# Optimization experiments

Measured on AMD Instinct MI355X. Metric: run time of the kernel, lower is better.

The kernel has to match this reference:

```python
import jax, jax.numpy as jnp
import numpy as np

WS = 8        # window_size
NH = 16       # num_heads

def setup_inputs() -> dict:
    key = jax.random.key(0)
    ks = jax.random.split(key, 6)
    B, H, W, C = 16, 64, 64, 512
    nW = (H // WS) * (W // WS)
    return {
        "x": jax.random.normal(ks[0], (B, H * W, C), jnp.float32),
        "qkv_w": jax.random.normal(ks[1], (3 * C, C), jnp.float32) * 0.02,
        "qkv_b": jax.random.normal(ks[2], (3 * C,), jnp.float32) * 0.02,
        "proj_w": jax.random.normal(ks[3], (C, C), jnp.float32) * 0.02,
        "proj_b": jax.random.normal(ks[4], (C,), jnp.float32) * 0.02,
        "attn_mask": jax.random.normal(ks[5], (nW, WS * WS, WS * WS), jnp.float32),
        "H": H,
        "W": W,
    }

def reference(x, qkv_w, qkv_b, proj_w, proj_b, attn_mask, H, W):
    B, N, C = x.shape
    ws = WS
    hd = C // NH
    scale = hd ** (-0.5)
    x_img = x.reshape(B, H, W, C)
    pad_h = (ws - H % ws) % ws
    pad_w = (ws - W % ws) % ws
    if pad_h > 0 or pad_w > 0:
        x_img = jnp.pad(x_img, ((0, 0), (0, pad_h), (0, pad_w), (0, 0)))
    Hp, Wp = H + pad_h, W + pad_w
    nW = (Hp // ws) * (Wp // ws)
    # window partition: [B*nW, ws*ws, C]
    x_win = x_img.reshape(B, Hp // ws, ws, Wp // ws, ws, C)
    x_win = x_win.transpose(0, 1, 3, 2, 4, 5).reshape(B * nW, ws * ws, C)
    # fused qkv projection (torch Linear: y = x @ W^T + b)
    qkv = x_win @ qkv_w.T + qkv_b
    qkv = qkv.reshape(B * nW, ws * ws, 3, NH, hd).transpose(2, 0, 3, 1, 4)
    q, k, v = qkv[0], qkv[1], qkv[2]  # each [B*nW, NH, ws*ws, hd]
    attn = jnp.einsum('bhqd,bhkd->bhqk', q, k) * scale
    if attn_mask is not None:
        attn = attn.reshape(B, nW, NH, ws * ws, ws * ws)
        attn = attn + attn_mask[None, :, None, :, :]
        attn = attn.reshape(B * nW, NH, ws * ws, ws * ws)
    attn = jax.nn.softmax(attn, axis=-1)
    out = jnp.einsum('bhqk,bhkd->bhqd', attn, v)
    out = out.transpose(0, 2, 1, 3).reshape(B * nW, ws * ws, C)
    out = out @ proj_w.T + proj_b
    # window reverse
    out = out.reshape(B, Hp // ws, Wp // ws, ws, ws, C)
    out = out.transpose(0, 1, 3, 2, 4, 5).reshape(B, Hp, Wp, C)
    out = out[:, :H, :W, :].reshape(B, H * W, C)
    return out
```

## Files before the change

kernel.cpp:

```cpp
#include <hip/hip_runtime.h>


typedef unsigned short u16;
typedef unsigned int u32;
typedef __attribute__((ext_vector_type(8))) u16 u16x8;
typedef __attribute__((ext_vector_type(8))) short short8;
typedef __attribute__((ext_vector_type(4))) float f32x4;

__device__ __forceinline__ u16 f2bf(float f) {
    u32 u = __float_as_uint(f);
    u += 0x7fffu + ((u >> 16) & 1u);
    return (u16)(u >> 16);
}

__device__ __forceinline__ f32x4 MFMA(u16x8 a, u16x8 b, f32x4 c) {
    return __builtin_amdgcn_mfma_f32_16x16x32_bf16(
        __builtin_bit_cast(short8, a), __builtin_bit_cast(short8, b), c, 0, 0, 0);
}

__device__ __forceinline__ void gload16(const void* g, void* l) {
    __builtin_amdgcn_global_load_lds(
        (const __attribute__((address_space(1))) void*)g,
        (__attribute__((address_space(3))) void*)l, 16, 0, 0);
}

__device__ __forceinline__ int win2img(int r) {
    int b = r >> 12;
    int w = (r >> 6) & 63;
    int t = r & 63;
    int img = (((w >> 3) << 3) + (t >> 3)) * 64 + ((w & 7) << 3) + (t & 7);
    return (b << 12) + img;
}

__device__ __forceinline__ u16x8 cvt8(const float* src) {
    float4 a = *(const float4*)src;
    float4 b = *(const float4*)(src + 4);
    u16x8 t;
    t[0] = f2bf(a.x); t[1] = f2bf(a.y); t[2] = f2bf(a.z); t[3] = f2bf(a.w);
    t[4] = f2bf(b.x); t[5] = f2bf(b.y); t[6] = f2bf(b.z); t[7] = f2bf(b.w);
    return t;
}

__global__ __launch_bounds__(256)
void conv_f2b(const float* __restrict__ in, u16* __restrict__ out, int n8) {
    int u = blockIdx.x * 256 + threadIdx.x;
    if (u >= n8) return;
    *(u16x8*)(out + (size_t)u * 8) = cvt8(in + (size_t)u * 8);
}

__global__ __launch_bounds__(256)
void conv_permute_x(const float* __restrict__ x, u16* __restrict__ xw) {
    int u = blockIdx.x * 256 + threadIdx.x;
    int r = u >> 6;
    int c = (u & 63) << 3;
    int g = win2img(r);
    *(u16x8*)(xw + (size_t)r * 512 + c) = cvt8(x + (size_t)g * 512 + c);
}

template<bool PERM_OUT, bool OUT_F32>
__global__ __launch_bounds__(512, 1)
void gemm8p(const u16* __restrict__ A, const u16* __restrict__ Wt,
            const float* __restrict__ bias, void* __restrict__ C,
            int NB, int Nfull)
{
    __shared__ char lds[131072];

    const int nwg = gridDim.x;
    const int q   = nwg >> 3;
    const int wg  = ((int)blockIdx.x & 7) * q + ((int)blockIdx.x >> 3);
    const int m0  = (wg / NB) * 256;
    const int n0  = (wg % NB) * 256;

    const int tid  = threadIdx.x;
    const int lane = tid & 63;
    const int wv   = tid >> 6;
    const int wm128 = (wv >> 2) << 7;
    const int wn64  = (wv & 3) << 6;
    const int lr = lane & 15;
    const int lg = lane >> 4;

    const int srow = tid >> 3;
    const int gcol = (((tid & 7) ^ (srow & 7)) << 4);
    const char* Ag = (const char*)A + (((size_t)(m0 + srow)) << 10) + gcol;
    const char* Bg = (const char*)Wt + (((size_t)(n0 + srow)) << 10) + gcol;
    const u32 stb = (u32)tid << 4;

    const int colx = (lr & 7) << 4;
    const u32 aro = (u32)(wm128 + lr) << 7;
    const u32 bro = (u32)(wn64 + lr) << 7;

    f32x4 acc[8][4] = {};
    u16x8 af[4], bf[4];

#define STG(buf, OP, h, kt) do {                                              \
    const char* g_ = (OP) ? Bg : Ag;                                          \
    char* d_ = lds + (buf) * 65536 + (OP) * 32768 + (h) * 16384 + stb;        \
    gload16(g_ + ((size_t)((h) * 128) << 10) + ((kt) << 7), d_);              \
    gload16(g_ + ((size_t)((h) * 128 + 64) << 10) + ((kt) << 7), d_ + 8192);  \
} while (0)

#define RDA(buf, h, s) do {                                                   \
    _Pragma("unroll") for (int j_ = 0; j_ < 4; ++j_)                          \
        af[j_] = *(const u16x8*)(lds + (buf) * 65536 + aro                    \
                   + (((h) * 4 + j_) << 11) + ((((s) << 6) + (lg << 4)) ^ colx)); \
} while (0)

#define RDB(buf, s) do {                                                      \
    _Pragma("unroll") for (int n_ = 0; n_ < 4; ++n_)                          \
        bf[n_] = *(const u16x8*)(lds + (buf) * 65536 + 32768 + bro            \
                   + (n_ << 11) + ((((s) << 6) + (lg << 4)) ^ colx));         \
} while (0)

#define MM16(h) do {                                                          \
    __builtin_amdgcn_s_setprio(1);                                            \
    _Pragma("unroll") for (int j_ = 0; j_ < 4; ++j_)                          \
        _Pragma("unroll") for (int n_ = 0; n_ < 4; ++n_)                      \
            acc[(h) * 4 + j_][n_] = MFMA(af[j_], bf[n_], acc[(h) * 4 + j_][n_]); \
    __builtin_amdgcn_s_setprio(0);                                            \
} while (0)

#define BAR() __builtin_amdgcn_s_barrier()
#define LGK0() do { asm volatile("s_waitcnt lgkmcnt(0)" ::: "memory");        \
                    __builtin_amdgcn_sched_barrier(0); } while (0)

    STG(0, 0, 0, 0); STG(0, 0, 1, 0); STG(0, 1, 0, 0); STG(0, 1, 1, 0);
    __syncthreads();

#pragma unroll
    for (int it = 0; it < 4; ++it) {
        const int t1 = 2 * it + 1, t2 = 2 * it + 2;
        RDA(0, 0, 0); RDB(0, 0);
        STG(1, 0, 0, t1); STG(1, 1, 0, t1);
        BAR(); LGK0(); MM16(0); BAR();
        RDA(0, 1, 0);
        STG(1, 0, 1, t1); STG(1, 1, 1, t1);
        BAR(); LGK0(); MM16(1); BAR();
        RDA(0, 0, 1); RDB(0, 1);
        BAR(); LGK0(); MM16(0); BAR();
        RDA(0, 1, 1);
        BAR(); LGK0(); MM16(1);
        __syncthreads();
        RDA(1, 0, 0); RDB(1, 0);
        if (it < 3) { STG(0, 0, 0, t2); STG(0, 1, 0, t2); }
        BAR(); LGK0(); MM16(0); BAR();
        RDA(1, 1, 0);
        if (it < 3) { STG(0, 0, 1, t2); STG(0, 1, 1, t2); }
        BAR(); LGK0(); MM16(1); BAR();
        RDA(1, 0, 1); RDB(1, 1);
        BAR(); LGK0(); MM16(0); BAR();
        RDA(1, 1, 1);
        BAR(); LGK0(); MM16(1);
        __syncthreads();
    }

#undef STG
#undef RDA
#undef RDB
#undef MM16
#undef BAR
#undef LGK0

#pragma unroll
    for (int ni = 0; ni < 4; ++ni) {
        const int col = n0 + wn64 + ni * 16 + lr;
        const float bv = bias[col];
#pragma unroll
        for (int mi = 0; mi < 8; ++mi) {
#pragma unroll
            for (int r = 0; r < 4; ++r) {
                int gr = m0 + wm128 + mi * 16 + lg * 4 + r;
                if (PERM_OUT) gr = win2img(gr);
                const float v = acc[mi][ni][r] + bv;
                if constexpr (OUT_F32)
                    ((float*)C)[(size_t)gr * Nfull + col] = v;
                else
                    ((u16*)C)[(size_t)gr * Nfull + col] = f2bf(v);
            }
        }
    }
}

__global__ __launch_bounds__(256, 2)
void attn_kernel(const u16* __restrict__ qkv, const float* __restrict__ mask,
                 u16* __restrict__ attn_out)
{
    __shared__ u16 sP[4][64][72];

    const int tid  = threadIdx.x;
    const int lane = tid & 63;
    const int wv   = tid >> 6;
    const int lr   = lane & 15;
    const int lg   = lane >> 4;
    const int win  = blockIdx.x;
    const int wib  = win & 63;
    const size_t rb = (size_t)win * 64;
    const float* maskp = mask + (size_t)wib * 64 * 64;
    const float scale = 0.17677669529663687f;

    for (int hi = 0; hi < 4; ++hi) {
        const int h = hi * 4 + wv;
        const size_t hoff = (size_t)h * 32;

        u16x8 qf[4], kf[4];
#pragma unroll
        for (int mt = 0; mt < 4; ++mt) {
            const u16* rowp = qkv + (rb + mt * 16 + lr) * 1536 + hoff + lg * 8;
            qf[mt] = *(const u16x8*)rowp;
            kf[mt] = *(const u16x8*)(rowp + 512);
        }
        f32x4 s[4][4] = {};
#pragma unroll
        for (int mi = 0; mi < 4; ++mi)
#pragma unroll
            for (int ni = 0; ni < 4; ++ni)
                s[mi][ni] = MFMA(qf[mi], kf[ni], s[mi][ni]);

        float rsum[4][4];
#pragma unroll
        for (int mi = 0; mi < 4; ++mi) {
#pragma unroll
            for (int r = 0; r < 4; ++r) {
                const int qrow = mi * 16 + lg * 4 + r;
                float vv[4];
                float mx = -1e30f;
#pragma unroll
                for (int ni = 0; ni < 4; ++ni) {
                    const int kcol = ni * 16 + lr;
                    float v = s[mi][ni][r] * scale + maskp[qrow * 64 + kcol];
                    vv[ni] = v;
                    mx = fmaxf(mx, v);
                }
#pragma unroll
                for (int mk = 1; mk <= 8; mk <<= 1)
                    mx = fmaxf(mx, __shfl_xor(mx, mk, 64));
                float sum = 0.f;
#pragma unroll
                for (int ni = 0; ni < 4; ++ni) {
                    float p = __expf(vv[ni] - mx);
                    sum += p;
                    s[mi][ni][r] = p;
                }
#pragma unroll
                for (int mk = 1; mk <= 8; mk <<= 1)
                    sum += __shfl_xor(sum, mk, 64);
                rsum[mi][r] = sum;
            }
        }

        __syncthreads();
#pragma unroll
        for (int mi = 0; mi < 4; ++mi)
#pragma unroll
            for (int ni = 0; ni < 4; ++ni)
#pragma unroll
                for (int r = 0; r < 4; ++r)
                    sP[wv][mi * 16 + lg * 4 + r][ni * 16 + lr] = f2bf(s[mi][ni][r]);
        __syncthreads();

        u16x8 pf[4][2];
#pragma unroll
        for (int mt = 0; mt < 4; ++mt)
#pragma unroll
            for (int k2 = 0; k2 < 2; ++k2)
                pf[mt][k2] = *(const u16x8*)&sP[wv][mt * 16 + lr][k2 * 32 + lg * 8];

        u16x8 vf[2][2];
#pragma unroll
        for (int k2 = 0; k2 < 2; ++k2)
#pragma unroll
            for (int nt = 0; nt < 2; ++nt) {
                const u16* vp = qkv + (rb + k2 * 32 + lg * 8) * 1536 + 1024 + hoff + nt * 16 + lr;
                u16x8 tmp;
#pragma unroll
                for (int j = 0; j < 8; ++j) tmp[j] = vp[(size_t)j * 1536];
                vf[k2][nt] = tmp;
            }

        f32x4 o[4][2] = {};
#pragma unroll
        for (int mt = 0; mt < 4; ++mt)
#pragma unroll
            for (int k2 = 0; k2 < 2; ++k2)
#pragma unroll
                for (int nt = 0; nt < 2; ++nt)
                    o[mt][nt] = MFMA(pf[mt][k2], vf[k2][nt], o[mt][nt]);

#pragma unroll
        for (int mt = 0; mt < 4; ++mt)
#pragma unroll
            for (int nt = 0; nt < 2; ++nt)
#pragma unroll
                for (int r = 0; r < 4; ++r) {
                    const int row = mt * 16 + lg * 4 + r;
                    const int d = nt * 16 + lr;
                    attn_out[(rb + row) * 512 + hoff + d] =
                        f2bf(o[mt][nt][r] / rsum[mt][r]);
                }
    }
}

extern "C" void kernel_launch(void* const* d_in, const int* in_sizes, int n_in,
                              void* d_out, int out_size, void* d_ws, size_t ws_size,
                              hipStream_t stream)
{
    const float* x      = (const float*)d_in[0];
    const float* qkv_w  = (const float*)d_in[1];
    const float* qkv_b  = (const float*)d_in[2];
    const float* proj_w = (const float*)d_in[3];
    const float* proj_b = (const float*)d_in[4];
    const float* mask   = (const float*)d_in[5];
    float* out = (float*)d_out;

    const size_t WQKV  = 1536ull * 512;
    const size_t WPROJ = 512ull * 512;

    u16* wq = (u16*)d_ws;
    u16* wp = wq + WQKV;
    u16* chunk = wp + WPROJ;

    const size_t xwPB  = 4096ull * 512;
    const size_t qkvPB = 4096ull * 1536;
    const size_t attPB = 4096ull * 512;
    const size_t perBatchBytes = (xwPB + qkvPB + attPB) * 2;

    size_t avail = ws_size - (WQKV + WPROJ) * 2;
    int Bc = (int)(avail / perBatchBytes);
    if (Bc > 16) Bc = 16;
    if (Bc < 1) Bc = 1;

    u16* xw_ws  = chunk;
    u16* qkv_ws = xw_ws + (size_t)Bc * xwPB;
    u16* att_ws = qkv_ws + (size_t)Bc * qkvPB;

    conv_f2b<<<dim3((WQKV / 8 + 255) / 256), 256, 0, stream>>>(qkv_w, wq, (int)(WQKV / 8));
    conv_f2b<<<dim3((WPROJ / 8 + 255) / 256), 256, 0, stream>>>(proj_w, wp, (int)(WPROJ / 8));

    for (int b0 = 0; b0 < 16; b0 += Bc) {
        const int bc = (16 - b0) < Bc ? (16 - b0) : Bc;
        const float* xc = x + (size_t)b0 * 4096 * 512;
        float* outc = out + (size_t)b0 * 4096 * 512;

        conv_permute_x<<<dim3(bc * 1024), 256, 0, stream>>>(xc, xw_ws);
        gemm8p<false, false><<<dim3(bc * 16 * 6), 512, 0, stream>>>(
            xw_ws, wq, qkv_b, qkv_ws, 6, 1536);
        attn_kernel<<<dim3(bc * 64), 256, 0, stream>>>(qkv_ws, mask, att_ws);
        gemm8p<true, true><<<dim3(bc * 16 * 2), 512, 0, stream>>>(
            att_ws, wp, proj_b, outc, 2, 512);
    }
}
```

Before: 347.6 us.

## Restructure GEMM mainloop to 4-slot ring of BK=32 tiles with prefetch depth two

Replaces the two-buffer BK=64 staging scheme with a four-slot LDS ring of BK=32 K-tiles, prefetching two tiles ahead and using vmcnt waits instead of full __syncthreads between stages. The LDS swizzle and load layout change to 64-byte rows with a 4-way XOR. The aim is to keep more global loads in flight and cut barrier stalls around the MFMA work. In exchange it uses more, finer-grained iterations and relies on tricky vmcnt accounting, which is a correctness risk.

Measured after the change: 357.4 us. 2.8% more time.

```diff
diff --git a/kernel.cpp b/kernel.cpp
--- a/kernel.cpp
+++ b/kernel.cpp
@@ -79,36 +79,36 @@
     const int lr = lane & 15;
     const int lg = lane >> 4;
 
-    const int srow = tid >> 3;
-    const int gcol = (((tid & 7) ^ (srow & 7)) << 4);
-    const char* Ag = (const char*)A + (((size_t)(m0 + srow)) << 10) + gcol;
-    const char* Bg = (const char*)Wt + (((size_t)(n0 + srow)) << 10) + gcol;
+    const int srow = tid >> 2;
+    const int gcolb = (((tid & 3) ^ ((tid >> 3) & 3)) << 4);
+    const char* Ag = (const char*)A + (((size_t)(m0 + srow)) << 10) + gcolb;
+    const char* Bg = (const char*)Wt + (((size_t)(n0 + srow)) << 10) + gcolb;
     const u32 stb = (u32)tid << 4;
 
-    const int colx = (lr & 7) << 4;
-    const u32 aro = (u32)(wm128 + lr) << 7;
-    const u32 bro = (u32)(wn64 + lr) << 7;
+    const u32 cbyte = (u32)((lg ^ ((lr >> 1) & 3)) << 4);
+    const u32 aoff = (u32)(wm128 + lr) * 64 + cbyte;
+    const u32 boff = (u32)(wn64 + lr) * 64 + cbyte + 16384;
 
     f32x4 acc[8][4] = {};
     u16x8 af[4], bf[4];
 
-#define STG(buf, OP, h, kt) do {                                              \
-    const char* g_ = (OP) ? Bg : Ag;                                          \
-    char* d_ = lds + (buf) * 65536 + (OP) * 32768 + (h) * 16384 + stb;        \
-    gload16(g_ + ((size_t)((h) * 128) << 10) + ((kt) << 7), d_);              \
-    gload16(g_ + ((size_t)((h) * 128 + 64) << 10) + ((kt) << 7), d_ + 8192);  \
-} while (0)
-
-#define RDA(buf, h, s) do {                                                   \
+#define STG(slot, kt) do {                                                    \
+    char* d_ = lds + (slot) * 32768 + stb;                                    \
+    const size_t ko_ = (size_t)(kt) << 6;                                     \
+    gload16(Ag + ko_,                d_);                                     \
+    gload16(Ag + (128 << 10) + ko_,  d_ + 8192);                              \
+    gload16(Bg + ko_,                d_ + 16384);                             \
+    gload16(Bg + (128 << 10) + ko_,  d_ + 24576);                             \
+} while (0)
+
+#define RDA(sb, h) do {                                                       \
     _Pragma("unroll") for (int j_ = 0; j_ < 4; ++j_)                          \
-        af[j_] = *(const u16x8*)(lds + (buf) * 65536 + aro                    \
-                   + (((h) * 4 + j_) << 11) + ((((s) << 6) + (lg << 4)) ^ colx)); \
-} while (0)
-
-#define RDB(buf, s) do {                                                      \
+        af[j_] = *(const u16x8*)(lds + (sb) + aoff + (((h) * 4 + j_) << 10)); \
+} while (0)
+
+#define RDB(sb) do {                                                          \
     _Pragma("unroll") for (int n_ = 0; n_ < 4; ++n_)                          \
-        bf[n_] = *(const u16x8*)(lds + (buf) * 65536 + 32768 + bro            \
-                   + (n_ << 11) + ((((s) << 6) + (lg << 4)) ^ colx));         \
+        bf[n_] = *(const u16x8*)(lds + (sb) + boff + (n_ << 10));             \
 } while (0)
 
 #define MM16(h) do {                                                          \
@@ -120,45 +120,43 @@
 } while (0)
 
 #define BAR() __builtin_amdgcn_s_barrier()
-#define LGK0() do { asm volatile("s_waitcnt lgkmcnt(0)" ::: "memory");        \
-                    __builtin_amdgcn_sched_barrier(0); } while (0)
-
-    STG(0, 0, 0, 0); STG(0, 0, 1, 0); STG(0, 1, 0, 0); STG(0, 1, 1, 0);
-    __syncthreads();
-
-#pragma unroll
-    for (int it = 0; it < 4; ++it) {
-        const int t1 = 2 * it + 1, t2 = 2 * it + 2;
-        RDA(0, 0, 0); RDB(0, 0);
-        STG(1, 0, 0, t1); STG(1, 1, 0, t1);
-        BAR(); LGK0(); MM16(0); BAR();
-        RDA(0, 1, 0);
-        STG(1, 0, 1, t1); STG(1, 1, 1, t1);
-        BAR(); LGK0(); MM16(1); BAR();
-        RDA(0, 0, 1); RDB(0, 1);
-        BAR(); LGK0(); MM16(0); BAR();
-        RDA(0, 1, 1);
-        BAR(); LGK0(); MM16(1);
-        __syncthreads();
-        RDA(1, 0, 0); RDB(1, 0);
-        if (it < 3) { STG(0, 0, 0, t2); STG(0, 1, 0, t2); }
-        BAR(); LGK0(); MM16(0); BAR();
-        RDA(1, 1, 0);
-        if (it < 3) { STG(0, 0, 1, t2); STG(0, 1, 1, t2); }
-        BAR(); LGK0(); MM16(1); BAR();
-        RDA(1, 0, 1); RDB(1, 1);
-        BAR(); LGK0(); MM16(0); BAR();
-        RDA(1, 1, 1);
-        BAR(); LGK0(); MM16(1);
-        __syncthreads();
+#define SB0() __builtin_amdgcn_sched_barrier(0)
+#define LGK0() do { asm volatile("s_waitcnt lgkmcnt(0)" ::: "memory"); SB0(); } while (0)
+#define VMC(n) do { asm volatile("s_waitcnt vmcnt(" #n ")" ::: "memory"); } while (0)
+
+    STG(0, 0);
+    STG(1, 1);
+
+#define TILE_BODY(t_, do_stg_)  do {                                          \
+    const int slot_ = (t_) & 3;                                               \
+    const int sb_ = slot_ * 32768;                                            \
+    BAR(); SB0();                                                             \
+    RDA(sb_, 0); RDB(sb_);                                                    \
+    if (do_stg_) STG(((t_) + 2) & 3, (t_) + 2);                               \
+    LGK0(); MM16(0); BAR();                                                   \
+    RDA(sb_, 1);                                                              \
+    LGK0(); MM16(1);                                                          \
+} while (0)
+
+#pragma unroll 2
+    for (int t = 0; t < 14; ++t) {
+        VMC(4);
+        TILE_BODY(t, 1);
     }
+    VMC(4); TILE_BODY(14, 0);
+    VMC(0); TILE_BODY(15, 0);
 
 #undef STG
 #undef RDA
 #undef RDB
 #undef MM16
 #undef BAR
+#undef SB0
 #undef LGK0
+#undef VMC
+#undef TILE_BODY
+
+    __syncthreads();
 
 #pragma unroll
     for (int ni = 0; ni < 4; ++ni) {
```
